# Kernel tuning notes

Hardware: AMD Instinct MI355X
Metric: run time of the kernel (lower is better)

The kernel has to match this reference:

```python
import jax, jax.numpy as jnp
import numpy as np

N_HEAD = 8

def _l2norm(x, eps=1e-12):
    # F.normalize(p=2, dim=-1): x / max(||x||_2, eps)
    return x / jnp.maximum(jnp.linalg.norm(x, axis=-1, keepdims=True), eps)

def setup_inputs() -> dict:
    key = jax.random.key(0)
    ks = jax.random.split(key, 9)
    B, L, E = 2, 2048, 512
    s = 0.02
    return {
        "query": jax.random.normal(ks[0], (B, L, E), dtype=jnp.float32),
        "Wq": s * jax.random.normal(ks[1], (E, E), dtype=jnp.float32),
        "bq": jnp.zeros((E,), dtype=jnp.float32),
        "Wk": s * jax.random.normal(ks[2], (E, E), dtype=jnp.float32),
        "bk": jnp.zeros((E,), dtype=jnp.float32),
        "Wv": s * jax.random.normal(ks[3], (E, E), dtype=jnp.float32),
        "bv": jnp.zeros((E,), dtype=jnp.float32),
        "Wo": s * jax.random.normal(ks[4], (E, E), dtype=jnp.float32),
        "bo": jnp.zeros((E,), dtype=jnp.float32),
    }

def reference(query, Wq, bq, Wk, bk, Wv, bv, Wo, bo):
    B, L, E = query.shape
    H = N_HEAD
    hd = E // H
    # Faithful to torch: .view(tgt_len, bsz, E) is a RESHAPE, not a transpose.
    x = query.reshape(L, B, E)
    q = jax.nn.relu(x @ Wq.T + bq)
    k = jax.nn.relu(x @ Wk.T + bk)
    v = x @ Wv.T + bv
    q = _l2norm(q)
    k = _l2norm(k)
    # (L, B, E) -> (L, B*H, hd) -> (B*H, L, hd)
    q_ = q.reshape(L, B * H, hd).transpose(1, 0, 2)
    k_ = k.reshape(L, B * H, hd).transpose(1, 0, 2)
    v_ = v.reshape(L, B * H, hd).transpose(1, 0, 2)
    # Causal linear attention: cumulative outer-product of k,v then contract with q.
    kv = jnp.einsum('nld,nlm->nldm', k_, v_)      # [B*H, L, hd, hd]
    kv_cum = jnp.cumsum(kv, axis=1)
    out = jnp.einsum('nld,nldm->nlm', q_, kv_cum)  # [B*H, L, hd]
    out = out.transpose(1, 0, 2).reshape(L, B, E)
    out = out @ Wo.T + bo
    return out.reshape(B, L, E)
```

## Files before the change

### kernel.cpp

```cpp
#include <hip/hip_runtime.h>
#include <hip/hip_bf16.h>

typedef __attribute__((ext_vector_type(8))) short short8;
typedef __attribute__((ext_vector_type(4))) float f32x4;
using bf16 = __hip_bfloat16;

__device__ __forceinline__ unsigned short f2bf(float f) {
    unsigned u = __float_as_uint(f);
    u += 0x7fff + ((u >> 16) & 1);
    return (unsigned short)(u >> 16);
}

__global__ __launch_bounds__(256) void cvt_kernel(
    const float* __restrict__ x, const float* __restrict__ wq, const float* __restrict__ wk,
    const float* __restrict__ wv, const float* __restrict__ wo,
    bf16* __restrict__ xb, bf16* __restrict__ wqb, bf16* __restrict__ wkb,
    bf16* __restrict__ wvb, bf16* __restrict__ wob)
{
    int y = blockIdx.y;
    const float* src; bf16* dst; int n;
    if (y == 0)      { src = x;  dst = xb;  n = 4096 * 512; }
    else if (y == 1) { src = wq; dst = wqb; n = 512 * 512; }
    else if (y == 2) { src = wk; dst = wkb; n = 512 * 512; }
    else if (y == 3) { src = wv; dst = wvb; n = 512 * 512; }
    else             { src = wo; dst = wob; n = 512 * 512; }
    int i4 = (blockIdx.x * 256 + threadIdx.x) * 4;
    if (i4 >= n) return;
    float4 v = *(const float4*)(src + i4);
    ushort4 u;
    u.x = f2bf(v.x); u.y = f2bf(v.y); u.z = f2bf(v.z); u.w = f2bf(v.w);
    *(ushort4*)((unsigned short*)dst + i4) = u;
}

template<int TN>
__global__ __launch_bounds__(256) void gemm_kernel(
    const bf16* __restrict__ A,
    const bf16* __restrict__ W0, const bf16* __restrict__ W1, const bf16* __restrict__ W2,
    const float* __restrict__ b0, const float* __restrict__ b1, const float* __restrict__ b2,
    float* __restrict__ O0, float* __restrict__ O1, float* __restrict__ O2,
    int nrelu)
{
    constexpr int NT = TN / 32;
    __shared__ bf16 As[64 * 40];
    __shared__ bf16 Bs[TN * 40];
    int z = blockIdx.z;
    const bf16* W = (z == 0) ? W0 : ((z == 1) ? W1 : W2);
    const float* bias = (z == 0) ? b0 : ((z == 1) ? b1 : b2);
    float* Out = (z == 0) ? O0 : ((z == 1) ? O1 : O2);
    bool relu = z < nrelu;

    int m0 = blockIdx.x * 64;
    int n0 = blockIdx.y * TN;
    int tid = threadIdx.x;
    int lane = tid & 63;
    int wave = tid >> 6;
    int wm = (wave >> 1) * 32;
    int wn = (wave & 1) * (TN / 2);

    f32x4 zero4 = {0.f, 0.f, 0.f, 0.f};
    f32x4 acc[2][NT];
    #pragma unroll
    for (int t = 0; t < 2; ++t)
        #pragma unroll
        for (int u = 0; u < NT; ++u) acc[t][u] = zero4;

    int srow = tid >> 2;
    int skk  = (tid & 3) * 8;

    for (int k0 = 0; k0 < 512; k0 += 32) {
        __syncthreads();
        *(uint4*)&As[srow * 40 + skk] = *(const uint4*)((const unsigned short*)A + (size_t)(m0 + srow) * 512 + k0 + skk);
        #pragma unroll
        for (int rep = 0; rep < TN / 64; ++rep) {
            int r = rep * 64 + srow;
            *(uint4*)&Bs[r * 40 + skk] = *(const uint4*)((const unsigned short*)W + (size_t)(n0 + r) * 512 + k0 + skk);
        }
        __syncthreads();
        int fr = lane & 15;
        int q  = lane >> 4;
        short8 af[2], bfr[NT];
        #pragma unroll
        for (int t = 0; t < 2; ++t) af[t] = *(const short8*)&As[(wm + t * 16 + fr) * 40 + q * 8];
        #pragma unroll
        for (int u = 0; u < NT; ++u) bfr[u] = *(const short8*)&Bs[(wn + u * 16 + fr) * 40 + q * 8];
        #pragma unroll
        for (int t = 0; t < 2; ++t)
            #pragma unroll
            for (int u = 0; u < NT; ++u)
                acc[t][u] = __builtin_amdgcn_mfma_f32_16x16x32_bf16(af[t], bfr[u], acc[t][u], 0, 0, 0);
    }

    int col = lane & 15;
    int rb  = (lane >> 4) * 4;
    #pragma unroll
    for (int t = 0; t < 2; ++t) {
        #pragma unroll
        for (int u = 0; u < NT; ++u) {
            int gn = n0 + wn + u * 16 + col;
            float bv = bias[gn];
            #pragma unroll
            for (int r = 0; r < 4; ++r) {
                int gm = m0 + wm + t * 16 + rb + r;
                float v = acc[t][u][r] + bv;
                if (relu) v = fmaxf(v, 0.f);
                Out[(size_t)gm * 512 + gn] = v;
            }
        }
    }
}

__global__ __launch_bounds__(256) void l2norm_kernel(
    const float* __restrict__ Qf, float* __restrict__ Kf,
    bf16* __restrict__ Qb, bf16* __restrict__ Kb)
{
    int row = blockIdx.x * 4 + (threadIdx.x >> 6);
    int lane = threadIdx.x & 63;
    bool isK = (blockIdx.y != 0);
    const float* src = (isK ? (const float*)Kf : Qf) + (size_t)row * 512;
    float4 a = ((const float4*)src)[lane];
    float4 cc = ((const float4*)src)[lane + 64];
    float s = a.x*a.x + a.y*a.y + a.z*a.z + a.w*a.w
            + cc.x*cc.x + cc.y*cc.y + cc.z*cc.z + cc.w*cc.w;
    #pragma unroll
    for (int off = 32; off > 0; off >>= 1) s += __shfl_xor(s, off, 64);
    float scale = 1.f / fmaxf(sqrtf(s), 1e-12f);
    a.x *= scale; a.y *= scale; a.z *= scale; a.w *= scale;
    cc.x *= scale; cc.y *= scale; cc.z *= scale; cc.w *= scale;
    unsigned short* dstb = (unsigned short*)(isK ? Kb : Qb) + (size_t)row * 512;
    ushort4 u0, u1;
    u0.x = f2bf(a.x);  u0.y = f2bf(a.y);  u0.z = f2bf(a.z);  u0.w = f2bf(a.w);
    u1.x = f2bf(cc.x); u1.y = f2bf(cc.y); u1.z = f2bf(cc.z); u1.w = f2bf(cc.w);
    *(ushort4*)&dstb[lane * 4] = u0;
    *(ushort4*)&dstb[256 + lane * 4] = u1;
    if (isK) {
        float* wb = Kf + (size_t)row * 512;
        ((float4*)wb)[lane] = a;
        ((float4*)wb)[lane + 64] = cc;
    }
}

__global__ __launch_bounds__(256) void chunk_kv_kernel(
    const float* __restrict__ Kf, const float* __restrict__ Vf,
    float* __restrict__ ScT, bf16* __restrict__ Vt_g)
{
    int n = blockIdx.x >> 4, c = blockIdx.x & 15;
    int b = n >> 3, h = n & 7;
    __shared__ float Ks[64 * 64];
    __shared__ float Vs[64 * 64];
    int tid = threadIdx.x;
    int td = tid >> 4, tm = tid & 15;
    int d0 = td * 4, m0 = tm * 4;
    int vm = tid & 63, vj0 = (tid >> 6) * 16;
    float acc[4][4] = {};
    for (int half = 0; half < 2; ++half) {
        __syncthreads();
        #pragma unroll
        for (int rep = 0; rep < 4; ++rep) {
            int idx = rep * 1024 + tid * 4;
            int j = idx >> 6, d = idx & 63;
            int grow = (c * 128 + half * 64 + j) * 2 + b;
            *(float4*)&Ks[j * 64 + d] = *(const float4*)&Kf[(size_t)grow * 512 + h * 64 + d];
            *(float4*)&Vs[j * 64 + d] = *(const float4*)&Vf[(size_t)grow * 512 + h * 64 + d];
        }
        __syncthreads();
        for (int j = 0; j < 64; ++j) {
            float4 kv = *(const float4*)&Ks[j * 64 + d0];
            float4 vv = *(const float4*)&Vs[j * 64 + m0];
            acc[0][0] += kv.x*vv.x; acc[0][1] += kv.x*vv.y; acc[0][2] += kv.x*vv.z; acc[0][3] += kv.x*vv.w;
            acc[1][0] += kv.y*vv.x; acc[1][1] += kv.y*vv.y; acc[1][2] += kv.y*vv.z; acc[1][3] += kv.y*vv.w;
            acc[2][0] += kv.z*vv.x; acc[2][1] += kv.z*vv.y; acc[2][2] += kv.z*vv.z; acc[2][3] += kv.z*vv.w;
            acc[3][0] += kv.w*vv.x; acc[3][1] += kv.w*vv.y; acc[3][2] += kv.w*vv.z; acc[3][3] += kv.w*vv.w;
        }
        unsigned short tmp[16];
        #pragma unroll
        for (int i = 0; i < 16; ++i) tmp[i] = f2bf(Vs[(vj0 + i) * 64 + vm]);
        size_t vtoff = (size_t)n * 131072 + (size_t)vm * 2048 + c * 128 + half * 64 + vj0;
        *(uint4*)((unsigned short*)Vt_g + vtoff)     = *(uint4*)&tmp[0];
        *(uint4*)((unsigned short*)Vt_g + vtoff + 8) = *(uint4*)&tmp[8];
    }
    float* outp = ScT + (size_t)blockIdx.x * 4096;
    #pragma unroll
    for (int j2 = 0; j2 < 4; ++j2) {
        float4 o4 = make_float4(acc[0][j2], acc[1][j2], acc[2][j2], acc[3][j2]);
        *(float4*)&outp[(m0 + j2) * 64 + d0] = o4;
    }
}

__global__ __launch_bounds__(256) void prefix_kernel(const float* __restrict__ ScT, bf16* __restrict__ SpT)
{
    int n = blockIdx.x >> 4;
    int idx = ((blockIdx.x & 15) << 8) + threadIdx.x;
    size_t base = (size_t)n * 65536 + idx;
    unsigned short* sp = (unsigned short*)SpT;
    float run = 0.f;
    #pragma unroll
    for (int c = 0; c < 16; ++c) {
        size_t off = base + (size_t)c * 4096;
        sp[off] = f2bf(run);
        run += ScT[off];
    }
}

__global__ __launch_bounds__(256) void attn_kernel(
    const bf16* __restrict__ Qb, const bf16* __restrict__ Kb,
    const bf16* __restrict__ Vt_g, const bf16* __restrict__ SpT_g,
    bf16* __restrict__ AOb)
{
    int n = blockIdx.x >> 4, c = blockIdx.x & 15;
    int b = n >> 3, h = n & 7;
    __shared__ unsigned short Qs[128 * 72];
    __shared__ unsigned short Ks[128 * 72];
    __shared__ unsigned short Vt[64 * 136];
    __shared__ unsigned short Ps[4 * 32 * 40];
    int tid = threadIdx.x;
    int lane = tid & 63;
    int w = tid >> 6;

    #pragma unroll
    for (int rep = 0; rep < 4; ++rep) {
        int idx = rep * 256 + tid;
        int l = idx >> 3, dc = (idx & 7) * 8;
        int grow = (c * 128 + l) * 2 + b;
        size_t goff = (size_t)grow * 512 + h * 64 + dc;
        *(uint4*)&Qs[l * 72 + dc] = *(const uint4*)((const unsigned short*)Qb + goff);
        *(uint4*)&Ks[l * 72 + dc] = *(const uint4*)((const unsigned short*)Kb + goff);
    }
    #pragma unroll
    for (int rep = 0; rep < 4; ++rep) {
        int idx = rep * 256 + tid;
        int m = idx >> 4, jc = (idx & 15) * 8;
        *(uint4*)&Vt[m * 136 + jc] =
            *(const uint4*)((const unsigned short*)Vt_g + (size_t)n * 131072 + (size_t)m * 2048 + c * 128 + jc);
    }
    __syncthreads();

    int fr = lane & 15, q = lane >> 4;
    short8 qf[2][2];
    #pragma unroll
    for (int lt = 0; lt < 2; ++lt)
        #pragma unroll
        for (int kh = 0; kh < 2; ++kh)
            qf[lt][kh] = *(const short8*)&Qs[(w * 32 + lt * 16 + fr) * 72 + kh * 32 + q * 8];

    f32x4 zero4 = {0.f, 0.f, 0.f, 0.f};
    f32x4 oacc[2][4];
    #pragma unroll
    for (int lt = 0; lt < 2; ++lt)
        #pragma unroll
        for (int mt = 0; mt < 4; ++mt) oacc[lt][mt] = zero4;

    const unsigned short* spg = (const unsigned short*)SpT_g + (size_t)blockIdx.x * 4096;
    #pragma unroll
    for (int mt = 0; mt < 4; ++mt) {
        #pragma unroll
        for (int kh = 0; kh < 2; ++kh) {
            short8 sf = *(const short8*)&spg[(mt * 16 + fr) * 64 + kh * 32 + q * 8];
            oacc[0][mt] = __builtin_amdgcn_mfma_f32_16x16x32_bf16(qf[0][kh], sf, oacc[0][mt], 0, 0, 0);
            oacc[1][mt] = __builtin_amdgcn_mfma_f32_16x16x32_bf16(qf[1][kh], sf, oacc[1][mt], 0, 0, 0);
        }
    }

    unsigned short* myPs = &Ps[w * 1280];
    int col = fr, rbase = q * 4;
    for (int jt = 0; jt <= w; ++jt) {
        f32x4 pacc[2][2];
        pacc[0][0] = zero4; pacc[0][1] = zero4; pacc[1][0] = zero4; pacc[1][1] = zero4;
        #pragma unroll
        for (int jt16 = 0; jt16 < 2; ++jt16) {
            #pragma unroll
            for (int kh = 0; kh < 2; ++kh) {
                short8 kf = *(const short8*)&Ks[(jt * 32 + jt16 * 16 + fr) * 72 + kh * 32 + q * 8];
                pacc[0][jt16] = __builtin_amdgcn_mfma_f32_16x16x32_bf16(qf[0][kh], kf, pacc[0][jt16], 0, 0, 0);
                pacc[1][jt16] = __builtin_amdgcn_mfma_f32_16x16x32_bf16(qf[1][kh], kf, pacc[1][jt16], 0, 0, 0);
            }
        }
        bool diag = (jt == w);
        #pragma unroll
        for (int lt = 0; lt < 2; ++lt)
            #pragma unroll
            for (int jt16 = 0; jt16 < 2; ++jt16)
                #pragma unroll
                for (int r = 0; r < 4; ++r) {
                    int ll = lt * 16 + rbase + r;
                    int jl = jt16 * 16 + col;
                    float pv = pacc[lt][jt16][r];
                    if (diag && jl > ll) pv = 0.f;
                    myPs[ll * 40 + jl] = f2bf(pv);
                }
        short8 pf0 = *(const short8*)&myPs[fr * 40 + q * 8];
        short8 pf1 = *(const short8*)&myPs[(16 + fr) * 40 + q * 8];
        #pragma unroll
        for (int mt = 0; mt < 4; ++mt) {
            short8 vf = *(const short8*)&Vt[(mt * 16 + fr) * 136 + jt * 32 + q * 8];
            oacc[0][mt] = __builtin_amdgcn_mfma_f32_16x16x32_bf16(pf0, vf, oacc[0][mt], 0, 0, 0);
            oacc[1][mt] = __builtin_amdgcn_mfma_f32_16x16x32_bf16(pf1, vf, oacc[1][mt], 0, 0, 0);
        }
    }

    __syncthreads();
    #pragma unroll
    for (int lt = 0; lt < 2; ++lt)
        #pragma unroll
        for (int mt = 0; mt < 4; ++mt)
            #pragma unroll
            for (int r = 0; r < 4; ++r)
                Qs[(w * 32 + lt * 16 + rbase + r) * 72 + mt * 16 + col] = f2bf(oacc[lt][mt][r]);
    __syncthreads();
    #pragma unroll
    for (int rep = 0; rep < 4; ++rep) {
        int idx = rep * 256 + tid;
        int l = idx >> 3, dc = (idx & 7) * 8;
        int grow = (c * 128 + l) * 2 + b;
        *(uint4*)((unsigned short*)AOb + (size_t)grow * 512 + h * 64 + dc) = *(const uint4*)&Qs[l * 72 + dc];
    }
}

extern "C" void kernel_launch(void* const* d_in, const int* in_sizes, int n_in,
                              void* d_out, int out_size, void* d_ws, size_t ws_size,
                              hipStream_t stream)
{
    (void)in_sizes; (void)n_in; (void)out_size; (void)ws_size;
    const float* x  = (const float*)d_in[0];
    const float* Wq = (const float*)d_in[1];
    const float* bq = (const float*)d_in[2];
    const float* Wk = (const float*)d_in[3];
    const float* bk = (const float*)d_in[4];
    const float* Wv = (const float*)d_in[5];
    const float* bv = (const float*)d_in[6];
    const float* Wo = (const float*)d_in[7];
    const float* bo = (const float*)d_in[8];
    float* out = (float*)d_out;

    bf16* Xb  = (bf16*)d_ws;
    bf16* Wqb = Xb + 2097152;
    bf16* Wkb = Wqb + 262144;
    bf16* Wvb = Wkb + 262144;
    bf16* Wob = Wvb + 262144;
    bf16* Qb  = Wob + 262144;
    bf16* Kb  = Qb + 2097152;
    bf16* Vt  = Kb + 2097152;
    bf16* SpT = Vt + 2097152;
    bf16* AOb = SpT + 1048576;
    float* Qf = (float*)(AOb + 2097152);
    float* Kf = Qf + 2097152;
    float* Vf = Kf + 2097152;
    float* ScT = Vf + 2097152;

    cvt_kernel<<<dim3(2048, 5), 256, 0, stream>>>(x, Wq, Wk, Wv, Wo, Xb, Wqb, Wkb, Wvb, Wob);
    gemm_kernel<128><<<dim3(64, 4, 3), 256, 0, stream>>>(Xb, Wqb, Wkb, Wvb, bq, bk, bv, Qf, Kf, Vf, 2);
    l2norm_kernel<<<dim3(1024, 2), 256, 0, stream>>>(Qf, Kf, Qb, Kb);
    chunk_kv_kernel<<<dim3(256), 256, 0, stream>>>(Kf, Vf, ScT, Vt);
    prefix_kernel<<<dim3(256), 256, 0, stream>>>(ScT, SpT);
    attn_kernel<<<dim3(256), 256, 0, stream>>>(Qb, Kb, Vt, SpT, AOb);
    gemm_kernel<64><<<dim3(64, 8, 1), 256, 0, stream>>>(AOb, Wob, Wob, Wob, bo, bo, bo, out, out, out, 0);
}
```

Before: 130.6 us.

## Fuse L2 norm into QKV GEMM via atomic row sums, drop prefix kernel

The QKV GEMM now writes bf16 outputs and accumulates per-row sums of squares with atomics. The normalization is deferred: the K scale is folded into V inside chunk_kv, and the Q scale is applied to the attention output. The separate l2norm and prefix kernels are removed, and attn now sums chunk states on the fly. GEMM and attention tiles are loaded with direct global-to-LDS loads in a k-major layout, and the output projection uses a 128x64 tile. This cuts fp32 intermediate traffic and kernel launches, but adds atomics, redundant prefix summation, and bf16 rounding of un-normalized K/V.

After: 161.2 us. +23.4%, slower.

```diff
diff --git a/kernel.cpp b/kernel.cpp
--- a/kernel.cpp
+++ b/kernel.cpp
@@ -10,14 +10,26 @@
     u += 0x7fff + ((u >> 16) & 1);
     return (unsigned short)(u >> 16);
 }
+__device__ __forceinline__ float bf2f(unsigned short s) {
+    return __uint_as_float(((unsigned)s) << 16);
+}
+__device__ __forceinline__ void gl_lds16(const unsigned short* g, unsigned short* l) {
+    __builtin_amdgcn_global_load_lds(
+        (const __attribute__((address_space(1))) unsigned int*)g,
+        (__attribute__((address_space(3))) unsigned int*)l, 16, 0, 0);
+}
 
 __global__ __launch_bounds__(256) void cvt_kernel(
     const float* __restrict__ x, const float* __restrict__ wq, const float* __restrict__ wk,
     const float* __restrict__ wv, const float* __restrict__ wo,
     bf16* __restrict__ xb, bf16* __restrict__ wqb, bf16* __restrict__ wkb,
-    bf16* __restrict__ wvb, bf16* __restrict__ wob)
+    bf16* __restrict__ wvb, bf16* __restrict__ wob, float* __restrict__ ssq)
 {
     int y = blockIdx.y;
+    if (y == 1 && blockIdx.x < 8) {
+        int zi = blockIdx.x * 1024 + threadIdx.x * 4;
+        *(float4*)&ssq[zi] = make_float4(0.f, 0.f, 0.f, 0.f);
+    }
     const float* src; bf16* dst; int n;
     if (y == 0)      { src = x;  dst = xb;  n = 4096 * 512; }
     else if (y == 1) { src = wq; dst = wqb; n = 512 * 512; }
@@ -32,121 +44,112 @@
     *(ushort4*)((unsigned short*)dst + i4) = u;
 }
 
-template<int TN>
-__global__ __launch_bounds__(256) void gemm_kernel(
+__global__ __launch_bounds__(256) void qkv_gemm_kernel(
     const bf16* __restrict__ A,
     const bf16* __restrict__ W0, const bf16* __restrict__ W1, const bf16* __restrict__ W2,
     const float* __restrict__ b0, const float* __restrict__ b1, const float* __restrict__ b2,
-    float* __restrict__ O0, float* __restrict__ O1, float* __restrict__ O2,
-    int nrelu)
-{
-    constexpr int NT = TN / 32;
-    __shared__ bf16 As[64 * 40];
-    __shared__ bf16 Bs[TN * 40];
+    bf16* __restrict__ O0, bf16* __restrict__ O1, bf16* __restrict__ O2,
+    float* __restrict__ ssq)
+{
+    __shared__ __align__(16) unsigned short smem[8192];
+    unsigned short* As = smem;
+    unsigned short* Bs = smem + 2048;
     int z = blockIdx.z;
-    const bf16* W = (z == 0) ? W0 : ((z == 1) ? W1 : W2);
+    const unsigned short* W = (const unsigned short*)((z == 0) ? W0 : ((z == 1) ? W1 : W2));
     const float* bias = (z == 0) ? b0 : ((z == 1) ? b1 : b2);
-    float* Out = (z == 0) ? O0 : ((z == 1) ? O1 : O2);
-    bool relu = z < nrelu;
+    unsigned short* Out = (unsigned short*)((z == 0) ? O0 : ((z == 1) ? O1 : O2));
+    const unsigned short* Ag = (const unsigned short*)A;
 
     int m0 = blockIdx.x * 64;
-    int n0 = blockIdx.y * TN;
+    int n0 = blockIdx.y * 128;
     int tid = threadIdx.x;
     int lane = tid & 63;
     int wave = tid >> 6;
     int wm = (wave >> 1) * 32;
-    int wn = (wave & 1) * (TN / 2);
+    int wn = (wave & 1) * 64;
+    int fr = lane & 15, q = lane >> 4;
 
     f32x4 zero4 = {0.f, 0.f, 0.f, 0.f};
-    f32x4 acc[2][NT];
+    f32x4 acc[2][4];
     #pragma unroll
     for (int t = 0; t < 2; ++t)
         #pragma unroll
-        for (int u = 0; u < NT; ++u) acc[t][u] = zero4;
-
-    int srow = tid >> 2;
-    int skk  = (tid & 3) * 8;
+        for (int u = 0; u < 4; ++u) acc[t][u] = zero4;
 
     for (int k0 = 0; k0 < 512; k0 += 32) {
         __syncthreads();
-        *(uint4*)&As[srow * 40 + skk] = *(const uint4*)((const unsigned short*)A + (size_t)(m0 + srow) * 512 + k0 + skk);
-        #pragma unroll
-        for (int rep = 0; rep < TN / 64; ++rep) {
-            int r = rep * 64 + srow;
-            *(uint4*)&Bs[r * 40 + skk] = *(const uint4*)((const unsigned short*)W + (size_t)(n0 + r) * 512 + k0 + skk);
-        }
-        __syncthreads();
-        int fr = lane & 15;
-        int q  = lane >> 4;
-        short8 af[2], bfr[NT];
-        #pragma unroll
-        for (int t = 0; t < 2; ++t) af[t] = *(const short8*)&As[(wm + t * 16 + fr) * 40 + q * 8];
-        #pragma unroll
-        for (int u = 0; u < NT; ++u) bfr[u] = *(const short8*)&Bs[(wn + u * 16 + fr) * 40 + q * 8];
+        gl_lds16(Ag + (size_t)(m0 + lane) * 512 + k0 + wave * 8, &As[wave * 512]);
+        #pragma unroll
+        for (int r = 0; r < 2; ++r)
+            gl_lds16(W + (size_t)(n0 + r * 64 + lane) * 512 + k0 + wave * 8,
+                     &Bs[(wave * 128 + r * 64) * 8]);
+        __syncthreads();
+        short8 af[2], bfr[4];
+        #pragma unroll
+        for (int t = 0; t < 2; ++t) af[t] = *(const short8*)&As[(q * 64 + wm + t * 16 + fr) * 8];
+        #pragma unroll
+        for (int u = 0; u < 4; ++u) bfr[u] = *(const short8*)&Bs[(q * 128 + wn + u * 16 + fr) * 8];
         #pragma unroll
         for (int t = 0; t < 2; ++t)
             #pragma unroll
-            for (int u = 0; u < NT; ++u)
+            for (int u = 0; u < 4; ++u)
                 acc[t][u] = __builtin_amdgcn_mfma_f32_16x16x32_bf16(af[t], bfr[u], acc[t][u], 0, 0, 0);
     }
 
-    int col = lane & 15;
-    int rb  = (lane >> 4) * 4;
-    #pragma unroll
-    for (int t = 0; t < 2; ++t) {
-        #pragma unroll
-        for (int u = 0; u < NT; ++u) {
-            int gn = n0 + wn + u * 16 + col;
-            float bv = bias[gn];
+    bool relu = (z < 2);
+    int rb = q * 4;
+    #pragma unroll
+    for (int t = 0; t < 2; ++t)
+        #pragma unroll
+        for (int u = 0; u < 4; ++u) {
+            float bv = bias[n0 + wn + u * 16 + fr];
             #pragma unroll
             for (int r = 0; r < 4; ++r) {
-                int gm = m0 + wm + t * 16 + rb + r;
                 float v = acc[t][u][r] + bv;
                 if (relu) v = fmaxf(v, 0.f);
-                Out[(size_t)gm * 512 + gn] = v;
+                acc[t][u][r] = v;
             }
         }
-    }
-}
-
-__global__ __launch_bounds__(256) void l2norm_kernel(
-    const float* __restrict__ Qf, float* __restrict__ Kf,
-    bf16* __restrict__ Qb, bf16* __restrict__ Kb)
-{
-    int row = blockIdx.x * 4 + (threadIdx.x >> 6);
-    int lane = threadIdx.x & 63;
-    bool isK = (blockIdx.y != 0);
-    const float* src = (isK ? (const float*)Kf : Qf) + (size_t)row * 512;
-    float4 a = ((const float4*)src)[lane];
-    float4 cc = ((const float4*)src)[lane + 64];
-    float s = a.x*a.x + a.y*a.y + a.z*a.z + a.w*a.w
-            + cc.x*cc.x + cc.y*cc.y + cc.z*cc.z + cc.w*cc.w;
-    #pragma unroll
-    for (int off = 32; off > 0; off >>= 1) s += __shfl_xor(s, off, 64);
-    float scale = 1.f / fmaxf(sqrtf(s), 1e-12f);
-    a.x *= scale; a.y *= scale; a.z *= scale; a.w *= scale;
-    cc.x *= scale; cc.y *= scale; cc.z *= scale; cc.w *= scale;
-    unsigned short* dstb = (unsigned short*)(isK ? Kb : Qb) + (size_t)row * 512;
-    ushort4 u0, u1;
-    u0.x = f2bf(a.x);  u0.y = f2bf(a.y);  u0.z = f2bf(a.z);  u0.w = f2bf(a.w);
-    u1.x = f2bf(cc.x); u1.y = f2bf(cc.y); u1.z = f2bf(cc.z); u1.w = f2bf(cc.w);
-    *(ushort4*)&dstb[lane * 4] = u0;
-    *(ushort4*)&dstb[256 + lane * 4] = u1;
-    if (isK) {
-        float* wb = Kf + (size_t)row * 512;
-        ((float4*)wb)[lane] = a;
-        ((float4*)wb)[lane + 64] = cc;
+    __syncthreads();
+    if (relu) {
+        #pragma unroll
+        for (int t = 0; t < 2; ++t)
+            #pragma unroll
+            for (int r = 0; r < 4; ++r) {
+                float s = 0.f;
+                #pragma unroll
+                for (int u = 0; u < 4; ++u) s += acc[t][u][r] * acc[t][u][r];
+                #pragma unroll
+                for (int off = 1; off < 16; off <<= 1) s += __shfl_xor(s, off, 64);
+                if (fr == 0) atomicAdd(&ssq[z * 4096 + m0 + wm + t * 16 + rb + r], s);
+            }
+    }
+    #pragma unroll
+    for (int t = 0; t < 2; ++t)
+        #pragma unroll
+        for (int u = 0; u < 4; ++u)
+            #pragma unroll
+            for (int r = 0; r < 4; ++r)
+                smem[(wm + t * 16 + rb + r) * 128 + wn + u * 16 + fr] = f2bf(acc[t][u][r]);
+    __syncthreads();
+    #pragma unroll
+    for (int rep = 0; rep < 4; ++rep) {
+        int idx8 = rep * 256 + tid;
+        int row = idx8 >> 4, col8 = (idx8 & 15) * 8;
+        *(uint4*)(Out + (size_t)(m0 + row) * 512 + n0 + col8) = *(const uint4*)&smem[row * 128 + col8];
     }
 }
 
 __global__ __launch_bounds__(256) void chunk_kv_kernel(
-    const float* __restrict__ Kf, const float* __restrict__ Vf,
-    float* __restrict__ ScT, bf16* __restrict__ Vt_g)
+    const bf16* __restrict__ Kb, const bf16* __restrict__ Vb,
+    const float* __restrict__ ssq, float* __restrict__ ScT, bf16* __restrict__ Vt_g)
 {
     int n = blockIdx.x >> 4, c = blockIdx.x & 15;
     int b = n >> 3, h = n & 7;
     __shared__ float Ks[64 * 64];
     __shared__ float Vs[64 * 64];
+    const unsigned short* Kg = (const unsigned short*)Kb;
+    const unsigned short* Vg = (const unsigned short*)Vb;
     int tid = threadIdx.x;
     int td = tid >> 4, tm = tid & 15;
     int d0 = td * 4, m0 = tm * 4;
@@ -159,8 +162,12 @@
             int idx = rep * 1024 + tid * 4;
             int j = idx >> 6, d = idx & 63;
             int grow = (c * 128 + half * 64 + j) * 2 + b;
-            *(float4*)&Ks[j * 64 + d] = *(const float4*)&Kf[(size_t)grow * 512 + h * 64 + d];
-            *(float4*)&Vs[j * 64 + d] = *(const float4*)&Vf[(size_t)grow * 512 + h * 64 + d];
+            ushort4 ku = *(const ushort4*)&Kg[(size_t)grow * 512 + h * 64 + d];
+            ushort4 vu = *(const ushort4*)&Vg[(size_t)grow * 512 + h * 64 + d];
+            float rk = 1.f / fmaxf(sqrtf(ssq[4096 + grow]), 1e-12f);
+            *(float4*)&Ks[j * 64 + d] = make_float4(bf2f(ku.x), bf2f(ku.y), bf2f(ku.z), bf2f(ku.w));
+            *(float4*)&Vs[j * 64 + d] = make_float4(bf2f(vu.x) * rk, bf2f(vu.y) * rk,
+                                                    bf2f(vu.z) * rk, bf2f(vu.w) * rk);
         }
         __syncthreads();
         for (int j = 0; j < 64; ++j) {
@@ -186,61 +193,45 @@
     }
 }
 
-__global__ __launch_bounds__(256) void prefix_kernel(const float* __restrict__ ScT, bf16* __restrict__ SpT)
-{
-    int n = blockIdx.x >> 4;
-    int idx = ((blockIdx.x & 15) << 8) + threadIdx.x;
-    size_t base = (size_t)n * 65536 + idx;
-    unsigned short* sp = (unsigned short*)SpT;
-    float run = 0.f;
-    #pragma unroll
-    for (int c = 0; c < 16; ++c) {
-        size_t off = base + (size_t)c * 4096;
-        sp[off] = f2bf(run);
-        run += ScT[off];
-    }
-}
-
 __global__ __launch_bounds__(256) void attn_kernel(
     const bf16* __restrict__ Qb, const bf16* __restrict__ Kb,
-    const bf16* __restrict__ Vt_g, const bf16* __restrict__ SpT_g,
-    bf16* __restrict__ AOb)
+    const bf16* __restrict__ Vt_g, const float* __restrict__ ScT,
+    const float* __restrict__ ssq, bf16* __restrict__ AOb)
 {
     int n = blockIdx.x >> 4, c = blockIdx.x & 15;
     int b = n >> 3, h = n & 7;
-    __shared__ unsigned short Qs[128 * 72];
-    __shared__ unsigned short Ks[128 * 72];
-    __shared__ unsigned short Vt[64 * 136];
+    __shared__ __align__(16) unsigned short Qs[8192];
+    __shared__ __align__(16) unsigned short Ks[8192];
+    __shared__ __align__(16) unsigned short Vt[8192];
     __shared__ unsigned short Ps[4 * 32 * 40];
     int tid = threadIdx.x;
     int lane = tid & 63;
     int w = tid >> 6;
-
-    #pragma unroll
-    for (int rep = 0; rep < 4; ++rep) {
-        int idx = rep * 256 + tid;
-        int l = idx >> 3, dc = (idx & 7) * 8;
-        int grow = (c * 128 + l) * 2 + b;
-        size_t goff = (size_t)grow * 512 + h * 64 + dc;
-        *(uint4*)&Qs[l * 72 + dc] = *(const uint4*)((const unsigned short*)Qb + goff);
-        *(uint4*)&Ks[l * 72 + dc] = *(const uint4*)((const unsigned short*)Kb + goff);
-    }
-    #pragma unroll
-    for (int rep = 0; rep < 4; ++rep) {
-        int idx = rep * 256 + tid;
-        int m = idx >> 4, jc = (idx & 15) * 8;
-        *(uint4*)&Vt[m * 136 + jc] =
-            *(const uint4*)((const unsigned short*)Vt_g + (size_t)n * 131072 + (size_t)m * 2048 + c * 128 + jc);
+    int fr = lane & 15, q = lane >> 4;
+
+    const unsigned short* Qg = (const unsigned short*)Qb;
+    const unsigned short* Kg = (const unsigned short*)Kb;
+    const unsigned short* Vg = (const unsigned short*)Vt_g;
+
+    #pragma unroll
+    for (int r = 0; r < 4; ++r) {
+        int id = w * 4 + r;
+        int dc = id >> 1, half = id & 1;
+        size_t go = (size_t)((c * 128 + half * 64 + lane) * 2 + b) * 512 + h * 64 + dc * 8;
+        gl_lds16(Qg + go, &Qs[(dc * 128 + half * 64) * 8]);
+        gl_lds16(Kg + go, &Ks[(dc * 128 + half * 64) * 8]);
+        int jc = id;
+        gl_lds16(Vg + (size_t)n * 131072 + (size_t)lane * 2048 + c * 128 + jc * 8,
+                 &Vt[jc * 64 * 8]);
     }
     __syncthreads();
 
-    int fr = lane & 15, q = lane >> 4;
     short8 qf[2][2];
     #pragma unroll
     for (int lt = 0; lt < 2; ++lt)
         #pragma unroll
         for (int kh = 0; kh < 2; ++kh)
-            qf[lt][kh] = *(const short8*)&Qs[(w * 32 + lt * 16 + fr) * 72 + kh * 32 + q * 8];
+            qf[lt][kh] = *(const short8*)&Qs[((kh * 4 + q) * 128 + w * 32 + lt * 16 + fr) * 8];
 
     f32x4 zero4 = {0.f, 0.f, 0.f, 0.f};
     f32x4 oacc[2][4];
@@ -249,19 +240,30 @@
         #pragma unroll
         for (int mt = 0; mt < 4; ++mt) oacc[lt][mt] = zero4;
 
-    const unsigned short* spg = (const unsigned short*)SpT_g + (size_t)blockIdx.x * 4096;
+    const float* scb = ScT + (size_t)(n * 16) * 4096;
     #pragma unroll
     for (int mt = 0; mt < 4; ++mt) {
         #pragma unroll
         for (int kh = 0; kh < 2; ++kh) {
-            short8 sf = *(const short8*)&spg[(mt * 16 + fr) * 64 + kh * 32 + q * 8];
+            float sp[8] = {0.f,0.f,0.f,0.f,0.f,0.f,0.f,0.f};
+            int eo = (mt * 16 + fr) * 64 + kh * 32 + q * 8;
+            for (int cp = 0; cp < c; ++cp) {
+                float4 a = *(const float4*)&scb[cp * 4096 + eo];
+                float4 d = *(const float4*)&scb[cp * 4096 + eo + 4];
+                sp[0]+=a.x; sp[1]+=a.y; sp[2]+=a.z; sp[3]+=a.w;
+                sp[4]+=d.x; sp[5]+=d.y; sp[6]+=d.z; sp[7]+=d.w;
+            }
+            unsigned short su[8];
+            #pragma unroll
+            for (int e = 0; e < 8; ++e) su[e] = f2bf(sp[e]);
+            short8 sf = *(const short8*)su;
             oacc[0][mt] = __builtin_amdgcn_mfma_f32_16x16x32_bf16(qf[0][kh], sf, oacc[0][mt], 0, 0, 0);
             oacc[1][mt] = __builtin_amdgcn_mfma_f32_16x16x32_bf16(qf[1][kh], sf, oacc[1][mt], 0, 0, 0);
         }
     }
 
     unsigned short* myPs = &Ps[w * 1280];
-    int col = fr, rbase = q * 4;
+    int rbase = q * 4;
     for (int jt = 0; jt <= w; ++jt) {
         f32x4 pacc[2][2];
         pacc[0][0] = zero4; pacc[0][1] = zero4; pacc[1][0] = zero4; pacc[1][1] = zero4;
@@ -269,7 +271,7 @@
         for (int jt16 = 0; jt16 < 2; ++jt16) {
             #pragma unroll
             for (int kh = 0; kh < 2; ++kh) {
-                short8 kf = *(const short8*)&Ks[(jt * 32 + jt16 * 16 + fr) * 72 + kh * 32 + q * 8];
+                short8 kf = *(const short8*)&Ks[((kh * 4 + q) * 128 + jt * 32 + jt16 * 16 + fr) * 8];
                 pacc[0][jt16] = __builtin_amdgcn_mfma_f32_16x16x32_bf16(qf[0][kh], kf, pacc[0][jt16], 0, 0, 0);
                 pacc[1][jt16] = __builtin_amdgcn_mfma_f32_16x16x32_bf16(qf[1][kh], kf, pacc[1][jt16], 0, 0, 0);
             }
@@ -282,7 +284,7 @@
                 #pragma unroll
                 for (int r = 0; r < 4; ++r) {
                     int ll = lt * 16 + rbase + r;
-                    int jl = jt16 * 16 + col;
+                    int jl = jt16 * 16 + fr;
                     float pv = pacc[lt][jt16][r];
                     if (diag && jl > ll) pv = 0.f;
                     myPs[ll * 40 + jl] = f2bf(pv);
@@ -291,12 +293,20 @@
         short8 pf1 = *(const short8*)&myPs[(16 + fr) * 40 + q * 8];
         #pragma unroll
         for (int mt = 0; mt < 4; ++mt) {
-            short8 vf = *(const short8*)&Vt[(mt * 16 + fr) * 136 + jt * 32 + q * 8];
+            short8 vf = *(const short8*)&Vt[((jt * 4 + q) * 64 + mt * 16 + fr) * 8];
             oacc[0][mt] = __builtin_amdgcn_mfma_f32_16x16x32_bf16(pf0, vf, oacc[0][mt], 0, 0, 0);
             oacc[1][mt] = __builtin_amdgcn_mfma_f32_16x16x32_bf16(pf1, vf, oacc[1][mt], 0, 0, 0);
         }
     }
 
+    float rqv[2][4];
+    #pragma unroll
+    for (int lt = 0; lt < 2; ++lt)
+        #pragma unroll
+        for (int r = 0; r < 4; ++r) {
+            int flat = (c * 128 + w * 32 + lt * 16 + rbase + r) * 2 + b;
+            rqv[lt][r] = 1.f / fmaxf(sqrtf(ssq[flat]), 1e-12f);
+        }
     __syncthreads();
     #pragma unroll
     for (int lt = 0; lt < 2; ++lt)
@@ -304,15 +314,73 @@
         for (int mt = 0; mt < 4; ++mt)
             #pragma unroll
             for (int r = 0; r < 4; ++r)
-                Qs[(w * 32 + lt * 16 + rbase + r) * 72 + mt * 16 + col] = f2bf(oacc[lt][mt][r]);
+                Qs[(w * 32 + lt * 16 + rbase + r) * 64 + mt * 16 + fr] = f2bf(oacc[lt][mt][r] * rqv[lt][r]);
     __syncthreads();
     #pragma unroll
     for (int rep = 0; rep < 4; ++rep) {
-        int idx = rep * 256 + tid;
-        int l = idx >> 3, dc = (idx & 7) * 8;
-        int grow = (c * 128 + l) * 2 + b;
-        *(uint4*)((unsigned short*)AOb + (size_t)grow * 512 + h * 64 + dc) = *(const uint4*)&Qs[l * 72 + dc];
-    }
+        int idx8 = rep * 256 + tid;
+        int l = idx8 >> 3, m8 = (idx8 & 7) * 8;
+        *(uint4*)((unsigned short*)AOb + (size_t)((c * 128 + l) * 2 + b) * 512 + h * 64 + m8) =
+            *(const uint4*)&Qs[l * 64 + m8];
+    }
+}
+
+__global__ __launch_bounds__(256) void oproj_kernel(
+    const bf16* __restrict__ A, const bf16* __restrict__ W,
+    const float* __restrict__ bias, float* __restrict__ Out)
+{
+    __shared__ __align__(16) unsigned short smem[6144];
+    unsigned short* As = smem;
+    unsigned short* Bs = smem + 4096;
+    const unsigned short* Ag = (const unsigned short*)A;
+    const unsigned short* Wg = (const unsigned short*)W;
+    int m0 = blockIdx.x * 128;
+    int n0 = blockIdx.y * 64;
+    int tid = threadIdx.x;
+    int lane = tid & 63;
+    int wave = tid >> 6;
+    int fr = lane & 15, q = lane >> 4;
+    int wm = (wave >> 1) * 64;
+    int wn = (wave & 1) * 32;
+
+    f32x4 zero4 = {0.f, 0.f, 0.f, 0.f};
+    f32x4 acc[4][2];
+    #pragma unroll
+    for (int t = 0; t < 4; ++t) { acc[t][0] = zero4; acc[t][1] = zero4; }
+
+    for (int k0 = 0; k0 < 512; k0 += 32) {
+        __syncthreads();
+        #pragma unroll
+        for (int r = 0; r < 2; ++r)
+            gl_lds16(Ag + (size_t)(m0 + r * 64 + lane) * 512 + k0 + wave * 8,
+                     &As[(wave * 128 + r * 64) * 8]);
+        gl_lds16(Wg + (size_t)(n0 + lane) * 512 + k0 + wave * 8, &Bs[wave * 64 * 8]);
+        __syncthreads();
+        short8 af[4], bf[2];
+        #pragma unroll
+        for (int t = 0; t < 4; ++t) af[t] = *(const short8*)&As[(q * 128 + wm + t * 16 + fr) * 8];
+        #pragma unroll
+        for (int u = 0; u < 2; ++u) bf[u] = *(const short8*)&Bs[(q * 64 + wn + u * 16 + fr) * 8];
+        #pragma unroll
+        for (int t = 0; t < 4; ++t)
+            #pragma unroll
+            for (int u = 0; u < 2; ++u)
+                acc[t][u] = __builtin_amdgcn_mfma_f32_16x16x32_bf16(af[t], bf[u], acc[t][u], 0, 0, 0);
+    }
+
+    int rb = q * 4;
+    #pragma unroll
+    for (int t = 0; t < 4; ++t)
+        #pragma unroll
+        for (int u = 0; u < 2; ++u) {
+            int gn = n0 + wn + u * 16 + fr;
+            float bv = bias[gn];
+            #pragma unroll
+            for (int r = 0; r < 4; ++r) {
+                int gm = m0 + wm + t * 16 + rb + r;
+                Out[(size_t)gm * 512 + gn] = acc[t][u][r] + bv;
+            }
+        }
 }
 
 extern "C" void kernel_launch(void* const* d_in, const int* in_sizes, int n_in,
@@ -331,26 +399,22 @@
     const float* bo = (const float*)d_in[8];
     float* out = (float*)d_out;
 
-    bf16* Xb  = (bf16*)d_ws;
+    float* ssq = (float*)d_ws;
+    bf16* Xb  = (bf16*)(ssq + 8192);
     bf16* Wqb = Xb + 2097152;
     bf16* Wkb = Wqb + 262144;
     bf16* Wvb = Wkb + 262144;
     bf16* Wob = Wvb + 262144;
     bf16* Qb  = Wob + 262144;
     bf16* Kb  = Qb + 2097152;
-    bf16* Vt  = Kb + 2097152;
-    bf16* SpT = Vt + 2097152;
-    bf16* AOb = SpT + 1048576;
-    float* Qf = (float*)(AOb + 2097152);
-    float* Kf = Qf + 2097152;
-    float* Vf = Kf + 2097152;
-    float* ScT = Vf + 2097152;
-
-    cvt_kernel<<<dim3(2048, 5), 256, 0, stream>>>(x, Wq, Wk, Wv, Wo, Xb, Wqb, Wkb, Wvb, Wob);
-    gemm_kernel<128><<<dim3(64, 4, 3), 256, 0, stream>>>(Xb, Wqb, Wkb, Wvb, bq, bk, bv, Qf, Kf, Vf, 2);
-    l2norm_kernel<<<dim3(1024, 2), 256, 0, stream>>>(Qf, Kf, Qb, Kb);
-    chunk_kv_kernel<<<dim3(256), 256, 0, stream>>>(Kf, Vf, ScT, Vt);
-    prefix_kernel<<<dim3(256), 256, 0, stream>>>(ScT, SpT);
-    attn_kernel<<<dim3(256), 256, 0, stream>>>(Qb, Kb, Vt, SpT, AOb);
-    gemm_kernel<64><<<dim3(64, 8, 1), 256, 0, stream>>>(AOb, Wob, Wob, Wob, bo, bo, bo, out, out, out, 0);
-}
+    bf16* Vb  = Kb + 2097152;
+    bf16* Vt  = Vb + 2097152;
+    bf16* AOb = Vt + 2097152;
+    float* ScT = (float*)(AOb + 2097152);
+
+    cvt_kernel<<<dim3(2048, 5), 256, 0, stream>>>(x, Wq, Wk, Wv, Wo, Xb, Wqb, Wkb, Wvb, Wob, ssq);
+    qkv_gemm_kernel<<<dim3(64, 4, 3), 256, 0, stream>>>(Xb, Wqb, Wkb, Wvb, bq, bk, bv, Qb, Kb, Vb, ssq);
+    chunk_kv_kernel<<<dim3(256), 256, 0, stream>>>(Kb, Vb, ssq, ScT, Vt);
+    attn_kernel<<<dim3(256), 256, 0, stream>>>(Qb, Kb, Vt, ScT, ssq, AOb);
+    oproj_kernel<<<dim3(32, 8), 256, 0, stream>>>(AOb, Wob, bo, out);
+}
```
